# Kernel optimization log

Hardware: AMD Instinct MI355X
Metric: run time of the kernel (lower is better)

## Reference

```python
import jax, jax.numpy as jnp
import numpy as np

BETA = 30.0


def setup_inputs() -> dict:
    key = jax.random.key(0)
    k_x, k1, k2, k3, kv = jax.random.split(key, 5)
    B, D = 4096, 128
    N = 32  # nodes per hidden layer
    VALUE_SCALE = 500.0
    return {
        "x": jax.random.normal(k_x, (B, D), dtype=jnp.float32),
        "W1": jax.random.normal(k1, (N, D), dtype=jnp.float32),
        "W2": jax.random.normal(k2, (N, D), dtype=jnp.float32),
        "W3": jax.random.normal(k3, (N, D), dtype=jnp.float32),
        "V": jax.random.normal(kv, (1, N, N, N), dtype=jnp.float32) / VALUE_SCALE,
    }


def reference(x, W1, W2, W3, V):
    # feat='sf': every gating layer reads the raw input x (h is never updated).
    # gate_i = sigmoid(beta * x @ W_i^T), shape [B, 32]
    g1 = jax.nn.sigmoid(BETA * (x @ W1.T))
    g2 = jax.nn.sigmoid(BETA * (x @ W2.T))
    g3 = jax.nn.sigmoid(BETA * (x @ W3.T))
    # prod='op': cp[b,i,j,k] = g1[b,i]*g2[b,j]*g3[b,k];
    # out[b] = sum_{ijk} cp[b,i,j,k] * V[0,i,j,k]  -- expressed as one contraction.
    return jnp.einsum("bi,bj,bk,ijk->b", g1, g2, g3, V[0])
```

## Files before the change

kernel.cpp:

```cpp
#include <hip/hip_runtime.h>


#define BETA 30.0f

typedef float v2f __attribute__((ext_vector_type(2)));

__device__ __forceinline__ float f4c(const float4 v, int c) {
    return c == 0 ? v.x : (c == 1 ? v.y : (c == 2 ? v.z : v.w));
}

__device__ __forceinline__ float qp_xor1(float a) {
    return __int_as_float(__builtin_amdgcn_mov_dpp(__float_as_int(a), 0xB1, 0xF, 0xF, true));
}
__device__ __forceinline__ float qp_xor2(float a) {
    return __int_as_float(__builtin_amdgcn_mov_dpp(__float_as_int(a), 0x4E, 0xF, 0xF, true));
}
__device__ __forceinline__ float dpp_half_mirror(float a) {
    return __int_as_float(__builtin_amdgcn_mov_dpp(__float_as_int(a), 0x141, 0xF, 0xF, true));
}
__device__ __forceinline__ float dpp_row_mirror(float a) {
    return __int_as_float(__builtin_amdgcn_mov_dpp(__float_as_int(a), 0x140, 0xF, 0xF, true));
}

__global__ __launch_bounds__(256, 2) void dlgn_v18_kernel(
    const float* __restrict__ x,
    const float* __restrict__ W1,
    const float* __restrict__ W2,
    const float* __restrict__ W3,
    const float* __restrict__ V,
    float* __restrict__ out)
{
    __shared__ float xlds[8 * 160];
    __shared__ float Gs[8][100];
    __shared__ float Plds[2560];

    const int t  = threadIdx.x;
    const int b0 = blockIdx.x * 8;

    {
        const int r    = t >> 5;
        const int col4 = t & 31;
        const float4 xv = ((const float4*)(x + (size_t)(b0 + r) * 128))[col4];
        const int skc = col4 >> 2, sc = col4 & 3;
        *(float4*)&xlds[r * 160 + skc * 20 + sc * 4] = xv;
    }

    const int fl = t >> 3;
    const int kc = t & 7;
    float4 w1c[4], w2c[4], w3c[4];
    {
        const float4* W1r = (const float4*)(W1 + fl * 128 + kc * 16);
        const float4* W2r = (const float4*)(W2 + fl * 128 + kc * 16);
        const float4* W3r = (const float4*)(W3 + fl * 128 + kc * 16);
#pragma unroll
        for (int c = 0; c < 4; ++c) {
            w1c[c] = W1r[c]; w2c[c] = W2r[c]; w3c[c] = W3r[c];
        }
    }
    __syncthreads();

    v2f acc2[3][8];
#pragma unroll
    for (int m = 0; m < 3; ++m)
#pragma unroll
        for (int r = 0; r < 8; ++r) acc2[m][r] = (v2f){0.f, 0.f};

#pragma unroll
    for (int r = 0; r < 8; ++r) {
        float4 xc[4];
#pragma unroll
        for (int c = 0; c < 4; ++c)
            xc[c] = *(const float4*)&xlds[r * 160 + kc * 20 + c * 4];
#pragma unroll
        for (int c = 0; c < 4; ++c) {
            const v2f xlo = (v2f){xc[c].x, xc[c].y};
            const v2f xhi = (v2f){xc[c].z, xc[c].w};
            acc2[0][r] = __builtin_elementwise_fma((v2f){w1c[c].x, w1c[c].y}, xlo, acc2[0][r]);
            acc2[0][r] = __builtin_elementwise_fma((v2f){w1c[c].z, w1c[c].w}, xhi, acc2[0][r]);
            acc2[1][r] = __builtin_elementwise_fma((v2f){w2c[c].x, w2c[c].y}, xlo, acc2[1][r]);
            acc2[1][r] = __builtin_elementwise_fma((v2f){w2c[c].z, w2c[c].w}, xhi, acc2[1][r]);
            acc2[2][r] = __builtin_elementwise_fma((v2f){w3c[c].x, w3c[c].y}, xlo, acc2[2][r]);
            acc2[2][r] = __builtin_elementwise_fma((v2f){w3c[c].z, w3c[c].w}, xhi, acc2[2][r]);
        }
    }

    const float4* V4 = (const float4*)V;
    float4 v[32];
#pragma unroll
    for (int i = 0; i < 32; ++i) v[i] = V4[i * 256 + t];

#pragma unroll
    for (int m = 0; m < 3; ++m) {
        float sel = 0.f;
#pragma unroll
        for (int r = 0; r < 8; ++r) {
            float a = acc2[m][r].x + acc2[m][r].y;
            a += qp_xor1(a);
            a += qp_xor2(a);
            a += dpp_half_mirror(a);
            if (kc == r) sel = a;
        }
        Gs[kc][32 * m + fl] = 1.0f / (1.0f + __expf(-BETA * sel));
    }
    __syncthreads();

    const int j  = t >> 3;
    const int c2 = t & 7;

    float p8[8];
#pragma unroll
    for (int b = 0; b < 8; ++b) {
        const float4* Gr = (const float4*)&Gs[b][0];
        float4 g1r[8];
#pragma unroll
        for (int c = 0; c < 8; ++c) g1r[c] = Gr[c];
        const float  g2s = Gs[b][32 + j];
        const float4 g3r = *(const float4*)&Gs[b][64 + c2 * 4];

        v2f u2a = (v2f){0.f, 0.f};
        v2f u2b = (v2f){0.f, 0.f};
#pragma unroll
        for (int i = 0; i < 32; ++i) {
            const float g1i = f4c(g1r[i >> 2], i & 3);
            const v2f g1v = (v2f){g1i, g1i};
            u2a = __builtin_elementwise_fma(g1v, (v2f){v[i].x, v[i].y}, u2a);
            u2b = __builtin_elementwise_fma(g1v, (v2f){v[i].z, v[i].w}, u2b);
        }
        float s = u2a.x * g3r.x;
        s = fmaf(u2a.y, g3r.y, s);
        s = fmaf(u2b.x, g3r.z, s);
        s = fmaf(u2b.y, g3r.w, s);
        p8[b] = s * g2s;
    }

    *(float4*)&Plds[t * 10]     = make_float4(p8[0], p8[1], p8[2], p8[3]);
    *(float4*)&Plds[t * 10 + 4] = make_float4(p8[4], p8[5], p8[6], p8[7]);
    __syncthreads();

    {
        const int fb2 = t >> 5;
        const int pt  = t & 31;
        float s = 0.f;
#pragma unroll
        for (int s8 = 0; s8 < 8; ++s8)
            s += Plds[(pt + s8 * 32) * 10 + fb2];
        s += qp_xor1(s);
        s += qp_xor2(s);
        s += dpp_half_mirror(s);
        s += dpp_row_mirror(s);
        s += __shfl_xor(s, 16);
        if (pt == 0) out[b0 + fb2] = s;
    }
}

extern "C" void kernel_launch(void* const* d_in, const int* in_sizes, int n_in,
                              void* d_out, int out_size, void* d_ws, size_t ws_size,
                              hipStream_t stream) {
    const float* x  = (const float*)d_in[0];
    const float* W1 = (const float*)d_in[1];
    const float* W2 = (const float*)d_in[2];
    const float* W3 = (const float*)d_in[3];
    const float* V  = (const float*)d_in[4];
    float* out = (float*)d_out;

    dlgn_v18_kernel<<<dim3(512), dim3(256), 0, stream>>>(x, W1, W2, W3, V, out);
}
```

Baseline: 12.43 us.

## Re-tile V contraction so each thread covers an 8x4x4 ijk block

Changes how the V tensor is split across threads. Before, each thread held all 32 i values for one j and four k. Now each thread holds 8 i, 4 j and 4 k values, with the j-gate applied inside the loop. This cuts the per-row LDS reads of gate vectors: four float4 loads replace eight float4 loads plus a scalar. It adds an extra FMA per j and changes the V global load pattern, which may hurt coalescing.

```diff
diff --git a/kernel.cpp b/kernel.cpp
--- a/kernel.cpp
+++ b/kernel.cpp
@@ -22,7 +22,7 @@
     return __int_as_float(__builtin_amdgcn_mov_dpp(__float_as_int(a), 0x140, 0xF, 0xF, true));
 }
 
-__global__ __launch_bounds__(256, 2) void dlgn_v18_kernel(
+__global__ __launch_bounds__(256, 2) void dlgn_v22_kernel(
     const float* __restrict__ x,
     const float* __restrict__ W1,
     const float* __restrict__ W2,
@@ -84,10 +84,15 @@
         }
     }
 
+    const int jg = (t >> 3) & 7;
+    const int ig = t >> 6;
     const float4* V4 = (const float4*)V;
     float4 v[32];
 #pragma unroll
-    for (int i = 0; i < 32; ++i) v[i] = V4[i * 256 + t];
+    for (int ii = 0; ii < 8; ++ii)
+#pragma unroll
+        for (int jj = 0; jj < 4; ++jj)
+            v[ii * 4 + jj] = V4[(ig * 8 + ii) * 256 + (jg * 4 + jj) * 8 + kc];
 
 #pragma unroll
     for (int m = 0; m < 3; ++m) {
@@ -104,33 +109,34 @@
     }
     __syncthreads();
 
-    const int j  = t >> 3;
-    const int c2 = t & 7;
-
     float p8[8];
 #pragma unroll
     for (int b = 0; b < 8; ++b) {
-        const float4* Gr = (const float4*)&Gs[b][0];
-        float4 g1r[8];
+        const float4 ga  = *(const float4*)&Gs[b][8 * ig];
+        const float4 gb  = *(const float4*)&Gs[b][8 * ig + 4];
+        const float4 g2r = *(const float4*)&Gs[b][32 + 4 * jg];
+        const float4 g3r = *(const float4*)&Gs[b][64 + 4 * kc];
+
+        float p = 0.f;
 #pragma unroll
-        for (int c = 0; c < 8; ++c) g1r[c] = Gr[c];
-        const float  g2s = Gs[b][32 + j];
-        const float4 g3r = *(const float4*)&Gs[b][64 + c2 * 4];
-
-        v2f u2a = (v2f){0.f, 0.f};
-        v2f u2b = (v2f){0.f, 0.f};
+        for (int jj = 0; jj < 4; ++jj) {
+            v2f wa = (v2f){0.f, 0.f};
+            v2f wb = (v2f){0.f, 0.f};
 #pragma unroll
-        for (int i = 0; i < 32; ++i) {
-            const float g1i = f4c(g1r[i >> 2], i & 3);
-            const v2f g1v = (v2f){g1i, g1i};
-            u2a = __builtin_elementwise_fma(g1v, (v2f){v[i].x, v[i].y}, u2a);
-            u2b = __builtin_elementwise_fma(g1v, (v2f){v[i].z, v[i].w}, u2b);
+            for (int ii = 0; ii < 8; ++ii) {
+                const float g1i = (ii < 4) ? f4c(ga, ii & 3) : f4c(gb, ii & 3);
+                const v2f g1v = (v2f){g1i, g1i};
+                const float4 vv = v[ii * 4 + jj];
+                wa = __builtin_elementwise_fma(g1v, (v2f){vv.x, vv.y}, wa);
+                wb = __builtin_elementwise_fma(g1v, (v2f){vv.z, vv.w}, wb);
+            }
+            float d = wa.x * g3r.x;
+            d = fmaf(wa.y, g3r.y, d);
+            d = fmaf(wb.x, g3r.z, d);
+            d = fmaf(wb.y, g3r.w, d);
+            p = fmaf(f4c(g2r, jj), d, p);
         }
-        float s = u2a.x * g3r.x;
-        s = fmaf(u2a.y, g3r.y, s);
-        s = fmaf(u2b.x, g3r.z, s);
-        s = fmaf(u2b.y, g3r.w, s);
-        p8[b] = s * g2s;
+        p8[b] = p;
     }
 
     *(float4*)&Plds[t * 10]     = make_float4(p8[0], p8[1], p8[2], p8[3]);
@@ -163,5 +169,5 @@
     const float* V  = (const float*)d_in[4];
     float* out = (float*)d_out;
 
-    dlgn_v18_kernel<<<dim3(512), dim3(256), 0, stream>>>(x, W1, W2, W3, V, out);
+    dlgn_v22_kernel<<<dim3(512), dim3(256), 0, stream>>>(x, W1, W2, W3, V, out);
 }
```

Result: slower. 16.28 us (+31.0%).
